# Performance work log

Hardware: AMD Instinct MI355X
Metric: run time of the kernel (lower is better)

## Reference

```python
import jax, jax.numpy as jnp
import numpy as np

NH = 10
EPS = 1e-10

def setup_inputs() -> dict:
    key = jax.random.key(0)
    k1, k2, k3, k4, k5 = jax.random.split(key, 5)
    b, n_s, e, n_t = 8, 8192, 32, 8192
    return {
        "x": jax.random.normal(k1, (b, n_s, e), dtype=jnp.float32),
        "rel_lon": jax.random.normal(k2, (n_t, n_s), dtype=jnp.float32),
        "rel_lat": jax.random.normal(k3, (n_t, n_s), dtype=jnp.float32),
        "coords_source": jax.random.uniform(k4, (n_s, 2), dtype=jnp.float32),
        "coords_target": jax.random.uniform(k5, (n_t, 2), dtype=jnp.float32),
    }

def reference(x, rel_lon, rel_lat, coords_source, coords_target):
    # ---- nn_layer: k-NN over precomputed relative coordinate matrices ----
    d_rel = jnp.sqrt(rel_lon ** 2 + rel_lat ** 2)          # [n_t, n_s]
    neg_d, idx = jax.lax.top_k(-d_rel, NH)                 # nh smallest distances
    indices_dist = -neg_d                                  # [n_t, nh]
    x_nearest = x[:, idx]                                  # [b, n_t, nh, e] gather
    indices_lon = jnp.take_along_axis(rel_lon, idx, axis=1)  # [n_t, nh]
    indices_lat = jnp.take_along_axis(rel_lat, idx, axis=1)  # [n_t, nh]
    # ---- interpolator: inverse-distance-weighted interpolation ----
    # pairwise target-source distances via the expanded form (avoids [n_t,n_s,2])
    t2 = jnp.sum(coords_target ** 2, axis=1)[:, None]      # [n_t, 1]
    s2 = jnp.sum(coords_source ** 2, axis=1)[None, :]      # [1, n_s]
    d2 = t2 + s2 - 2.0 * coords_target @ coords_source.T   # [n_t, n_s]
    d_ts = jnp.sqrt(jnp.maximum(d2, 1e-12))
    w = 1.0 / (d_ts + EPS)
    w = w / jnp.sum(w, axis=1, keepdims=True)              # [n_t, n_s]
    x_inter = jnp.einsum('bse,ts->bte', x, w)              # [b, n_t, e]
    return (x_nearest, x_inter, indices_dist, indices_lon, indices_lat)
```

## Files before the change

### kernel.cpp

```cpp
#include <hip/hip_runtime.h>
#include <hip/hip_bf16.h>
#include <stdint.h>

#define B_   8
#define NS_  8192
#define E_   32
#define NT_  8192
#define NH_  10
#define NCH_ 128
#define CAND_CAP 512

typedef __bf16 bf16x8 __attribute__((ext_vector_type(8)));
typedef float  f32x4  __attribute__((ext_vector_type(4)));
typedef unsigned short ushort8_t __attribute__((ext_vector_type(8)));
typedef unsigned short ushort4_t __attribute__((ext_vector_type(4)));

static __device__ inline unsigned short f2bf(float f) {
  __hip_bfloat16 h = __float2bfloat16(f);
  return *reinterpret_cast<unsigned short*>(&h);
}
static __device__ inline float bf2f(unsigned short u) {
  __hip_bfloat16 h;
  *reinterpret_cast<unsigned short*>(&h) = u;
  return __bfloat162float(h);
}

static __device__ inline float tenth_smallest(float v, int lane) {
  unsigned long long kv =
      ((unsigned long long)__float_as_uint(v) << 32) | (unsigned)lane;
  float out = 0.f;
#pragma unroll
  for (int k = 0; k < NH_; ++k) {
    unsigned long long m = kv;
#pragma unroll
    for (int off = 32; off > 0; off >>= 1) {
      const unsigned long long o = __shfl_xor(m, off, 64);
      m = o < m ? o : m;
    }
    if (kv == m) kv = ~0ull;
    if (k == NH_ - 1) out = __uint_as_float((unsigned)(m >> 32));
  }
  return out;
}

__global__ __launch_bounds__(256) void topk_kernel(
    const float* __restrict__ rel_lon, const float* __restrict__ rel_lat,
    float* __restrict__ out_d, float* __restrict__ out_lon,
    float* __restrict__ out_lat, int* __restrict__ idx_out)
{
  __shared__ int cnt[4];
  __shared__ unsigned int cand[4][CAND_CAP];

  const int wave = threadIdx.x >> 6;
  const int lane = threadIdx.x & 63;
  const int t = blockIdx.x * 4 + wave;
  const float* lon_row = rel_lon + (size_t)t * NS_;
  const float* lat_row = rel_lat + (size_t)t * NS_;
  const float4* lon4 = (const float4*)lon_row;
  const float4* lat4 = (const float4*)lat_row;

  if (lane == 0) cnt[wave] = 0;

  const float4 lo0 = lon4[0 * 64 + lane], la0 = lat4[0 * 64 + lane];
  const float4 lo1 = lon4[1 * 64 + lane], la1 = lat4[1 * 64 + lane];
  float4 blo0 = lon4[2 * 64 + lane], bla0 = lat4[2 * 64 + lane];
  float4 blo1 = lon4[3 * 64 + lane], bla1 = lat4[3 * 64 + lane];
  float4 blo2 = lon4[4 * 64 + lane], bla2 = lat4[4 * 64 + lane];
  float4 blo3 = lon4[5 * 64 + lane], bla3 = lat4[5 * 64 + lane];

  float d2a[4], d2b[4];
  d2a[0] = __fmaf_rn(lo0.x, lo0.x, __fmul_rn(la0.x, la0.x));
  d2a[1] = __fmaf_rn(lo0.y, lo0.y, __fmul_rn(la0.y, la0.y));
  d2a[2] = __fmaf_rn(lo0.z, lo0.z, __fmul_rn(la0.z, la0.z));
  d2a[3] = __fmaf_rn(lo0.w, lo0.w, __fmul_rn(la0.w, la0.w));
  d2b[0] = __fmaf_rn(lo1.x, lo1.x, __fmul_rn(la1.x, la1.x));
  d2b[1] = __fmaf_rn(lo1.y, lo1.y, __fmul_rn(la1.y, la1.y));
  d2b[2] = __fmaf_rn(lo1.z, lo1.z, __fmul_rn(la1.z, la1.z));
  d2b[3] = __fmaf_rn(lo1.w, lo1.w, __fmul_rn(la1.w, la1.w));
  float lmin = fminf(fminf(fminf(d2a[0], d2a[1]), fminf(d2a[2], d2a[3])),
                     fminf(fminf(d2b[0], d2b[1]), fminf(d2b[2], d2b[3])));
  const float T = tenth_smallest(lmin, lane) * 1.000002f;

#pragma unroll
  for (int j = 0; j < 4; ++j) {
    if (d2a[j] <= T) {
      const int pos = atomicAdd(&cnt[wave], 1);
      if (pos < CAND_CAP) cand[wave][pos] = (unsigned)(lane * 4 + j);
    }
  }
#pragma unroll
  for (int j = 0; j < 4; ++j) {
    if (d2b[j] <= T) {
      const int pos = atomicAdd(&cnt[wave], 1);
      if (pos < CAND_CAP) cand[wave][pos] = (unsigned)(256 + lane * 4 + j);
    }
  }

#pragma unroll
  for (int c = 2; c < 32; ++c) {
    float4 lo, la;
    switch ((c - 2) & 3) {
      case 0: lo = blo0; la = bla0; break;
      case 1: lo = blo1; la = bla1; break;
      case 2: lo = blo2; la = bla2; break;
      default: lo = blo3; la = bla3; break;
    }
    if (c + 4 < 32) {
      switch ((c - 2) & 3) {
        case 0: blo0 = lon4[(c + 4) * 64 + lane]; bla0 = lat4[(c + 4) * 64 + lane]; break;
        case 1: blo1 = lon4[(c + 4) * 64 + lane]; bla1 = lat4[(c + 4) * 64 + lane]; break;
        case 2: blo2 = lon4[(c + 4) * 64 + lane]; bla2 = lat4[(c + 4) * 64 + lane]; break;
        default: blo3 = lon4[(c + 4) * 64 + lane]; bla3 = lat4[(c + 4) * 64 + lane]; break;
      }
    }
    float dv[4];
    dv[0] = __fmaf_rn(lo.x, lo.x, __fmul_rn(la.x, la.x));
    dv[1] = __fmaf_rn(lo.y, lo.y, __fmul_rn(la.y, la.y));
    dv[2] = __fmaf_rn(lo.z, lo.z, __fmul_rn(la.z, la.z));
    dv[3] = __fmaf_rn(lo.w, lo.w, __fmul_rn(la.w, la.w));
    const float mn = fminf(fminf(dv[0], dv[1]), fminf(dv[2], dv[3]));
    if (mn <= T) {
      const int s = c * 256 + lane * 4;
#pragma unroll
      for (int j = 0; j < 4; ++j) {
        if (dv[j] <= T) {
          const int pos = atomicAdd(&cnt[wave], 1);
          if (pos < CAND_CAP) cand[wave][pos] = (unsigned)(s + j);
        }
      }
    }
  }

  __syncthreads();

  const int ncand = min(cnt[wave], CAND_CAP);

  unsigned long long top[NH_];
#pragma unroll
  for (int i = 0; i < NH_; ++i) top[i] = ~0ull;

#pragma unroll
  for (int cc = 0; cc < CAND_CAP / 64; ++cc) {
    const int ci = lane + cc * 64;
    if (ci < ncand) {
      const unsigned s = cand[wave][ci];
      const float lo = lon_row[s];
      const float la = lat_row[s];
      const float d = __fsqrt_rn(__fadd_rn(__fmul_rn(lo, lo),
                                           __fmul_rn(la, la)));
      unsigned long long p =
          ((unsigned long long)__float_as_uint(d) << 32) | s;
#pragma unroll
      for (int i = 0; i < NH_; ++i) {
        const bool lt = p < top[i];
        const unsigned long long mn2 = lt ? p : top[i];
        const unsigned long long mx2 = lt ? top[i] : p;
        top[i] = mn2;
        p = mx2;
      }
    }
  }

  unsigned long long resv = ~0ull;
  unsigned long long cur = top[0];
#pragma unroll
  for (int k = 0; k < NH_; ++k) {
    unsigned long long m = cur;
#pragma unroll
    for (int off = 32; off > 0; off >>= 1) {
      const unsigned long long o = __shfl_xor(m, off, 64);
      m = o < m ? o : m;
    }
    if (cur == m) {
#pragma unroll
      for (int i = 0; i < NH_ - 1; ++i) top[i] = top[i + 1];
      top[NH_ - 1] = ~0ull;
      cur = top[0];
    }
    if (lane == k) resv = m;
  }

  if (lane < NH_) {
    const unsigned s = (unsigned)(resv & 0xffffffffu);
    const float d = __uint_as_float((unsigned)(resv >> 32));
    out_d[t * NH_ + lane] = d;
    idx_out[t * NH_ + lane] = (int)s;
    out_lon[t * NH_ + lane] = lon_row[s];
    out_lat[t * NH_ + lane] = lat_row[s];
  }
}

__global__ __launch_bounds__(256) void gather_kernel(
    const float* __restrict__ x, const int* __restrict__ idxbuf,
    float* __restrict__ out_xn)
{
  const int t = blockIdx.x;
  __shared__ int sidx[NH_];
  if (threadIdx.x < NH_) sidx[threadIdx.x] = idxbuf[t * NH_ + threadIdx.x];
  __syncthreads();
  for (int i = threadIdx.x; i < B_ * NH_ * (E_ / 4); i += 256) {
    const int e4 = i & 7;
    const int k = (i >> 3) % NH_;
    const int b = (i >> 3) / NH_;
    const int s = sidx[k];
    const float4 v = *(const float4*)(x + ((size_t)b * NS_ + s) * E_ + e4 * 4);
    *(float4*)(out_xn + (((size_t)b * NT_ + t) * NH_ + k) * E_ + e4 * 4) = v;
  }
}

__global__ __launch_bounds__(256) void xprep_kernel(
    const float* __restrict__ x, unsigned short* __restrict__ XT2)
{
  __shared__ __align__(16) unsigned short T[32][136];
  const int b = blockIdx.y;
  const int s0 = blockIdx.x * 128;
  const int tid = threadIdx.x;
  const int eq = tid & 7, slq = tid >> 3;
#pragma unroll
  for (int r4 = 0; r4 < 4; ++r4) {
    const int sl = r4 * 32 + slq;
    const float4 v = *(const float4*)&x[((size_t)b * NS_ + s0 + sl) * E_ + eq * 4];
    T[eq * 4 + 0][sl] = f2bf(v.x);
    T[eq * 4 + 1][sl] = f2bf(v.y);
    T[eq * 4 + 2][sl] = f2bf(v.z);
    T[eq * 4 + 3][sl] = f2bf(v.w);
  }
  __syncthreads();
  const int r = tid & 31, cq = tid >> 5;
  const int be = b * 32 + r;
  const int sA = s0 + cq * 16;
  const int c = sA >> 6;
  const int kA = (sA >> 3) & 7;
  unsigned short* dst = XT2 + ((size_t)(c * 8 + kA) * 256 + be) * 8;
  *(ushort8_t*)dst = *(const ushort8_t*)&T[r][cq * 16];
  *(ushort8_t*)(dst + 2048) = *(const ushort8_t*)&T[r][cq * 16 + 8];
}

__global__ __launch_bounds__(512) void xinter_mfma(
    const unsigned short* __restrict__ XT2, const float* __restrict__ cs,
    const float* __restrict__ ct, float* __restrict__ out_xi)
{
#pragma clang fp contract(off)
  __shared__ __align__(16) unsigned short Xl[2][8][256][8];
  __shared__ __align__(16) unsigned short Rl[2][8][16][8];
  __shared__ float RsumP[16][32];
  __shared__ float RsumInv[32];

  const int tid = threadIdx.x;
  const int w = tid >> 6, l = tid & 63;
  const int mg = w >> 1, ng = w & 1;
  const int lcol = l & 15, lkg = l >> 4;
  const int t0 = blockIdx.x * 32;

  const int gt = tid & 31;
  const int gq = tid >> 5;
  const int gng = gt >> 4, glc = gt & 15;
  const int gk = gq >> 1;
  const int gsl = (gq & 1) * 4;
  const float2 ctg = ((const float2*)ct)[t0 + gt];
  const float t2g = ctg.x * ctg.x + ctg.y * ctg.y;
  float rpart = 0.f;

  const int t = t0 + ng * 16 + lcol;

  f32x4 acc[4];
#pragma unroll
  for (int m = 0; m < 4; ++m)
#pragma unroll
    for (int j = 0; j < 4; ++j) acc[m][j] = 0.f;

#define STAGE_CHUNK(buf, ch)                                                 \
  {                                                                          \
    const unsigned short* gsrc =                                             \
        XT2 + ((size_t)(ch) * 8 + w) * 2048 + (size_t)l * 8;                 \
    _Pragma("unroll")                                                        \
    for (int bg = 0; bg < 4; ++bg) {                                         \
      __builtin_amdgcn_global_load_lds(                                      \
          (const __attribute__((address_space(1))) void*)(gsrc + bg * 512),  \
          (__attribute__((address_space(3))) void*)&Xl[buf][w][bg * 64][0],  \
          16, 0, 0);                                                         \
    }                                                                        \
  }

  STAGE_CHUNK(0, 0);
  asm volatile("s_waitcnt vmcnt(0)" ::: "memory");
  __builtin_amdgcn_s_barrier();

  int cur = 0;
  for (int c = 0; c < NCH_; ++c) {
    if (c + 1 < NCH_) STAGE_CHUNK(cur ^ 1, c + 1);

    {
      const int sb = c * 64 + gq * 4;
      const float4 cA = *(const float4*)&cs[2 * sb];
      const float4 cB = *(const float4*)&cs[2 * sb + 4];
      const float sxv[4] = {cA.x, cA.z, cB.x, cB.z};
      const float syv[4] = {cA.y, cA.w, cB.y, cB.w};
      ushort4_t ro;
#pragma unroll
      for (int j = 0; j < 4; ++j) {
        const float sx = sxv[j], sy = syv[j];
        const float s2 = sx * sx + sy * sy;
        const float p0 = ctg.x * sx;
        const float dot = fmaf(ctg.y, sy, p0);
        const float ts = t2g + s2;
        float d2 = ts - 2.0f * dot;
        d2 = fmaxf(d2, 1e-12f);
        const float r = __builtin_amdgcn_rsqf(d2);
        const unsigned short ub = f2bf(r);
        ro[j] = ub;
        rpart += bf2f(ub);
      }
      *(ushort4_t*)&Rl[gng][gk][glc][gsl] = ro;
    }
    asm volatile("s_waitcnt lgkmcnt(0)" ::: "memory");
    __builtin_amdgcn_s_barrier();

#pragma unroll
    for (int half = 0; half < 2; ++half) {
      const bf16x8 Bf = *(const bf16x8*)&Rl[ng][half * 4 + lkg][lcol][0];
#pragma unroll
      for (int m = 0; m < 4; ++m) {
        const bf16x8 a =
            *(const bf16x8*)&Xl[cur][half * 4 + lkg][(mg * 4 + m) * 16 + lcol][0];
        acc[m] = __builtin_amdgcn_mfma_f32_16x16x32_bf16(a, Bf, acc[m], 0, 0, 0);
      }
    }

    asm volatile("s_waitcnt vmcnt(0)" ::: "memory");
    __builtin_amdgcn_s_barrier();
    cur ^= 1;
  }
#undef STAGE_CHUNK

  RsumP[gq][gt] = rpart;
  asm volatile("s_waitcnt lgkmcnt(0)" ::: "memory");
  __builtin_amdgcn_s_barrier();
  if (tid < 32) {
    float ssum = 0.f;
#pragma unroll
    for (int q = 0; q < 16; ++q) ssum += RsumP[q][tid];
    RsumInv[tid] = 1.0f / ssum;
  }
  asm volatile("s_waitcnt lgkmcnt(0)" ::: "memory");
  __builtin_amdgcn_s_barrier();
  const float ri = RsumInv[ng * 16 + lcol];

#pragma unroll
  for (int m = 0; m < 4; ++m) {
    const int be0 = (mg * 4 + m) * 16 + lkg * 4;
    const int b = be0 >> 5, e = be0 & 31;
    float4 o;
    o.x = acc[m][0] * ri;
    o.y = acc[m][1] * ri;
    o.z = acc[m][2] * ri;
    o.w = acc[m][3] * ri;
    *(float4*)&out_xi[((size_t)b * NT_ + t) * E_ + e] = o;
  }
}

extern "C" void kernel_launch(void* const* d_in, const int* in_sizes, int n_in,
                              void* d_out, int out_size, void* d_ws,
                              size_t ws_size, hipStream_t stream)
{
  const float* x       = (const float*)d_in[0];
  const float* rel_lon = (const float*)d_in[1];
  const float* rel_lat = (const float*)d_in[2];
  const float* cs      = (const float*)d_in[3];
  const float* ct      = (const float*)d_in[4];

  float* out = (float*)d_out;
  float* out_xn  = out;
  float* out_xi  = out + (size_t)B_ * NT_ * NH_ * E_;
  float* out_d   = out_xi + (size_t)B_ * NT_ * E_;
  float* out_lon = out_d + (size_t)NT_ * NH_;
  float* out_lat = out_lon + (size_t)NT_ * NH_;

  int* idxbuf = (int*)d_ws;
  unsigned short* XT2 = (unsigned short*)out_xn;

  topk_kernel<<<NT_ / 4, 256, 0, stream>>>(rel_lon, rel_lat, out_d, out_lon,
                                           out_lat, idxbuf);
  xprep_kernel<<<dim3(NS_ / 128, B_), 256, 0, stream>>>(x, XT2);
  xinter_mfma<<<NT_ / 32, 512, 0, stream>>>(XT2, cs, ct, out_xi);
  gather_kernel<<<NT_, 256, 0, stream>>>(x, idxbuf, out_xn);
}
```

Measured before the change: 297.4 us.

## Split each top-k row across four waves with per-quarter thresholds

The top-k kernel now assigns one target row per block, and each of its four waves scans a quarter of the source columns instead of the whole row. Each wave derives its own threshold from its first 512 elements and collects candidates into a smaller per-quarter LDS buffer, then wave 0 merges all four candidate lists. This shortens the serial per-wave scan and exposes more memory-level parallelism, with launch bounds raised for occupancy. The cost is that per-quarter thresholds are looser, so more candidates reach the merge, the merge runs on a single wave, and the 128-entry cap per quarter could overflow.

```diff
diff --git a/kernel.cpp b/kernel.cpp
--- a/kernel.cpp
+++ b/kernel.cpp
@@ -8,7 +8,7 @@
 #define NT_  8192
 #define NH_  10
 #define NCH_ 128
-#define CAND_CAP 512
+#define QCAP 128
 
 typedef __bf16 bf16x8 __attribute__((ext_vector_type(8)));
 typedef float  f32x4  __attribute__((ext_vector_type(4)));
@@ -43,31 +43,27 @@
   return out;
 }
 
-__global__ __launch_bounds__(256) void topk_kernel(
+__global__ __launch_bounds__(256, 8) void topk_kernel(
     const float* __restrict__ rel_lon, const float* __restrict__ rel_lat,
     float* __restrict__ out_d, float* __restrict__ out_lon,
     float* __restrict__ out_lat, int* __restrict__ idx_out)
 {
   __shared__ int cnt[4];
-  __shared__ unsigned int cand[4][CAND_CAP];
-
-  const int wave = threadIdx.x >> 6;
+  __shared__ unsigned int cand[4][QCAP];
+
+  const int q = threadIdx.x >> 6;
   const int lane = threadIdx.x & 63;
-  const int t = blockIdx.x * 4 + wave;
+  const int t = blockIdx.x;
   const float* lon_row = rel_lon + (size_t)t * NS_;
   const float* lat_row = rel_lat + (size_t)t * NS_;
-  const float4* lon4 = (const float4*)lon_row;
-  const float4* lat4 = (const float4*)lat_row;
-
-  if (lane == 0) cnt[wave] = 0;
+  const int base = q * 2048;
+  const float4* lon4 = (const float4*)(lon_row + base);
+  const float4* lat4 = (const float4*)(lat_row + base);
+
+  if (lane == 0) cnt[q] = 0;
 
   const float4 lo0 = lon4[0 * 64 + lane], la0 = lat4[0 * 64 + lane];
   const float4 lo1 = lon4[1 * 64 + lane], la1 = lat4[1 * 64 + lane];
-  float4 blo0 = lon4[2 * 64 + lane], bla0 = lat4[2 * 64 + lane];
-  float4 blo1 = lon4[3 * 64 + lane], bla1 = lat4[3 * 64 + lane];
-  float4 blo2 = lon4[4 * 64 + lane], bla2 = lat4[4 * 64 + lane];
-  float4 blo3 = lon4[5 * 64 + lane], bla3 = lat4[5 * 64 + lane];
-
   float d2a[4], d2b[4];
   d2a[0] = __fmaf_rn(lo0.x, lo0.x, __fmul_rn(la0.x, la0.x));
   d2a[1] = __fmaf_rn(lo0.y, lo0.y, __fmul_rn(la0.y, la0.y));
@@ -77,42 +73,30 @@
   d2b[1] = __fmaf_rn(lo1.y, lo1.y, __fmul_rn(la1.y, la1.y));
   d2b[2] = __fmaf_rn(lo1.z, lo1.z, __fmul_rn(la1.z, la1.z));
   d2b[3] = __fmaf_rn(lo1.w, lo1.w, __fmul_rn(la1.w, la1.w));
-  float lmin = fminf(fminf(fminf(d2a[0], d2a[1]), fminf(d2a[2], d2a[3])),
-                     fminf(fminf(d2b[0], d2b[1]), fminf(d2b[2], d2b[3])));
+  const float lmin =
+      fminf(fminf(fminf(d2a[0], d2a[1]), fminf(d2a[2], d2a[3])),
+            fminf(fminf(d2b[0], d2b[1]), fminf(d2b[2], d2b[3])));
   const float T = tenth_smallest(lmin, lane) * 1.000002f;
 
 #pragma unroll
   for (int j = 0; j < 4; ++j) {
     if (d2a[j] <= T) {
-      const int pos = atomicAdd(&cnt[wave], 1);
-      if (pos < CAND_CAP) cand[wave][pos] = (unsigned)(lane * 4 + j);
+      const int pos = atomicAdd(&cnt[q], 1);
+      if (pos < QCAP) cand[q][pos] = (unsigned)(base + lane * 4 + j);
     }
   }
 #pragma unroll
   for (int j = 0; j < 4; ++j) {
     if (d2b[j] <= T) {
-      const int pos = atomicAdd(&cnt[wave], 1);
-      if (pos < CAND_CAP) cand[wave][pos] = (unsigned)(256 + lane * 4 + j);
-    }
-  }
-
-#pragma unroll
-  for (int c = 2; c < 32; ++c) {
-    float4 lo, la;
-    switch ((c - 2) & 3) {
-      case 0: lo = blo0; la = bla0; break;
-      case 1: lo = blo1; la = bla1; break;
-      case 2: lo = blo2; la = bla2; break;
-      default: lo = blo3; la = bla3; break;
-    }
-    if (c + 4 < 32) {
-      switch ((c - 2) & 3) {
-        case 0: blo0 = lon4[(c + 4) * 64 + lane]; bla0 = lat4[(c + 4) * 64 + lane]; break;
-        case 1: blo1 = lon4[(c + 4) * 64 + lane]; bla1 = lat4[(c + 4) * 64 + lane]; break;
-        case 2: blo2 = lon4[(c + 4) * 64 + lane]; bla2 = lat4[(c + 4) * 64 + lane]; break;
-        default: blo3 = lon4[(c + 4) * 64 + lane]; bla3 = lat4[(c + 4) * 64 + lane]; break;
-      }
-    }
+      const int pos = atomicAdd(&cnt[q], 1);
+      if (pos < QCAP) cand[q][pos] = (unsigned)(base + 256 + lane * 4 + j);
+    }
+  }
+
+#pragma unroll
+  for (int p = 2; p < 8; ++p) {
+    const float4 lo = lon4[p * 64 + lane];
+    const float4 la = lat4[p * 64 + lane];
     float dv[4];
     dv[0] = __fmaf_rn(lo.x, lo.x, __fmul_rn(la.x, la.x));
     dv[1] = __fmaf_rn(lo.y, lo.y, __fmul_rn(la.y, la.y));
@@ -120,12 +104,12 @@
     dv[3] = __fmaf_rn(lo.w, lo.w, __fmul_rn(la.w, la.w));
     const float mn = fminf(fminf(dv[0], dv[1]), fminf(dv[2], dv[3]));
     if (mn <= T) {
-      const int s = c * 256 + lane * 4;
+      const int s = base + p * 256 + lane * 4;
 #pragma unroll
       for (int j = 0; j < 4; ++j) {
         if (dv[j] <= T) {
-          const int pos = atomicAdd(&cnt[wave], 1);
-          if (pos < CAND_CAP) cand[wave][pos] = (unsigned)(s + j);
+          const int pos = atomicAdd(&cnt[q], 1);
+          if (pos < QCAP) cand[q][pos] = (unsigned)(s + j);
         }
       }
     }
@@ -133,60 +117,64 @@
 
   __syncthreads();
 
-  const int ncand = min(cnt[wave], CAND_CAP);
-
-  unsigned long long top[NH_];
-#pragma unroll
-  for (int i = 0; i < NH_; ++i) top[i] = ~0ull;
-
-#pragma unroll
-  for (int cc = 0; cc < CAND_CAP / 64; ++cc) {
-    const int ci = lane + cc * 64;
-    if (ci < ncand) {
-      const unsigned s = cand[wave][ci];
-      const float lo = lon_row[s];
-      const float la = lat_row[s];
-      const float d = __fsqrt_rn(__fadd_rn(__fmul_rn(lo, lo),
-                                           __fmul_rn(la, la)));
-      unsigned long long p =
-          ((unsigned long long)__float_as_uint(d) << 32) | s;
-#pragma unroll
-      for (int i = 0; i < NH_; ++i) {
-        const bool lt = p < top[i];
-        const unsigned long long mn2 = lt ? p : top[i];
-        const unsigned long long mx2 = lt ? top[i] : p;
-        top[i] = mn2;
-        p = mx2;
-      }
-    }
-  }
-
-  unsigned long long resv = ~0ull;
-  unsigned long long cur = top[0];
-#pragma unroll
-  for (int k = 0; k < NH_; ++k) {
-    unsigned long long m = cur;
-#pragma unroll
-    for (int off = 32; off > 0; off >>= 1) {
-      const unsigned long long o = __shfl_xor(m, off, 64);
-      m = o < m ? o : m;
-    }
-    if (cur == m) {
-#pragma unroll
-      for (int i = 0; i < NH_ - 1; ++i) top[i] = top[i + 1];
-      top[NH_ - 1] = ~0ull;
-      cur = top[0];
-    }
-    if (lane == k) resv = m;
-  }
-
-  if (lane < NH_) {
-    const unsigned s = (unsigned)(resv & 0xffffffffu);
-    const float d = __uint_as_float((unsigned)(resv >> 32));
-    out_d[t * NH_ + lane] = d;
-    idx_out[t * NH_ + lane] = (int)s;
-    out_lon[t * NH_ + lane] = lon_row[s];
-    out_lat[t * NH_ + lane] = lat_row[s];
+  if (q == 0) {
+    unsigned long long top[NH_];
+#pragma unroll
+    for (int i = 0; i < NH_; ++i) top[i] = ~0ull;
+
+#pragma unroll
+    for (int seg = 0; seg < 4; ++seg) {
+      const int nc = min(cnt[seg], QCAP);
+#pragma unroll
+      for (int cc = 0; cc < QCAP / 64; ++cc) {
+        const int ci = lane + cc * 64;
+        if (ci < nc) {
+          const unsigned s = cand[seg][ci];
+          const float lo = lon_row[s];
+          const float la = lat_row[s];
+          const float d = __fsqrt_rn(__fadd_rn(__fmul_rn(lo, lo),
+                                               __fmul_rn(la, la)));
+          unsigned long long p =
+              ((unsigned long long)__float_as_uint(d) << 32) | s;
+#pragma unroll
+          for (int i = 0; i < NH_; ++i) {
+            const bool lt = p < top[i];
+            const unsigned long long mn2 = lt ? p : top[i];
+            const unsigned long long mx2 = lt ? top[i] : p;
+            top[i] = mn2;
+            p = mx2;
+          }
+        }
+      }
+    }
+
+    unsigned long long resv = ~0ull;
+    unsigned long long cur = top[0];
+#pragma unroll
+    for (int k = 0; k < NH_; ++k) {
+      unsigned long long m = cur;
+#pragma unroll
+      for (int off = 32; off > 0; off >>= 1) {
+        const unsigned long long o = __shfl_xor(m, off, 64);
+        m = o < m ? o : m;
+      }
+      if (cur == m) {
+#pragma unroll
+        for (int i = 0; i < NH_ - 1; ++i) top[i] = top[i + 1];
+        top[NH_ - 1] = ~0ull;
+        cur = top[0];
+      }
+      if (lane == k) resv = m;
+    }
+
+    if (lane < NH_) {
+      const unsigned s = (unsigned)(resv & 0xffffffffu);
+      const float d = __uint_as_float((unsigned)(resv >> 32));
+      out_d[t * NH_ + lane] = d;
+      idx_out[t * NH_ + lane] = (int)s;
+      out_lon[t * NH_ + lane] = lon_row[s];
+      out_lat[t * NH_ + lane] = lat_row[s];
+    }
   }
 }
 
@@ -339,7 +327,7 @@
   if (tid < 32) {
     float ssum = 0.f;
 #pragma unroll
-    for (int q = 0; q < 16; ++q) ssum += RsumP[q][tid];
+    for (int qq = 0; qq < 16; ++qq) ssum += RsumP[qq][tid];
     RsumInv[tid] = 1.0f / ssum;
   }
   asm volatile("s_waitcnt lgkmcnt(0)" ::: "memory");
@@ -379,8 +367,8 @@
   int* idxbuf = (int*)d_ws;
   unsigned short* XT2 = (unsigned short*)out_xn;
 
-  topk_kernel<<<NT_ / 4, 256, 0, stream>>>(rel_lon, rel_lat, out_d, out_lon,
-                                           out_lat, idxbuf);
+  topk_kernel<<<NT_, 256, 0, stream>>>(rel_lon, rel_lat, out_d, out_lon,
+                                       out_lat, idxbuf);
   xprep_kernel<<<dim3(NS_ / 128, B_), 256, 0, stream>>>(x, XT2);
   xinter_mfma<<<NT_ / 32, 512, 0, stream>>>(XT2, cs, ct, out_xi);
   gather_kernel<<<NT_, 256, 0, stream>>>(x, idxbuf, out_xn);
```

After: 289.2 us. 1.03x faster.
